# Kernel tuning notes

Hardware: AMD Instinct MI355X
Metric: run time of the kernel (lower is better)

## Reference

```python
import jax, jax.numpy as jnp
import numpy as np

B, S, E, H = 4, 2048, 1024, 16
D = E // H  # key_size


def setup_inputs() -> dict:
    key = jax.random.key(0)
    ks = jax.random.split(key, 6)
    s = 1.0 / np.sqrt(E)
    return {
        "X": jax.random.normal(ks[0], (B, S, E), dtype=jnp.float32),
        "Wq": jax.random.uniform(ks[1], (E, E), jnp.float32, -s, s),
        "Wk": jax.random.uniform(ks[2], (E, E), jnp.float32, -s, s),
        "Wv": jax.random.uniform(ks[3], (E, E), jnp.float32, -s, s),
        "Wo": jax.random.uniform(ks[4], (E, E), jnp.float32, -s, s),
        "bo": jax.random.uniform(ks[5], (E,), jnp.float32, -s, s),
    }


def reference(X, Wq, Wk, Wv, Wo, bo):
    # Linear layers: y = x @ W^T (torch convention), no bias for q/k/v
    def split(x):  # [B,S,E] -> [B,H,S,D]
        return x.reshape(B, S, H, D).transpose(0, 2, 1, 3)

    q = split(X @ Wq.T)
    k = split(X @ Wk.T)
    v = split(X @ Wv.T)
    scale = jnp.asarray(np.sqrt(D), dtype=X.dtype)
    scores = jnp.einsum("bhqd,bhkd->bhqk", q, k) / scale
    probs = jax.nn.softmax(scores, axis=-1)
    ctx = jnp.einsum("bhqk,bhkd->bhqd", probs, v)
    out = ctx.transpose(0, 2, 1, 3).reshape(B, S, E)
    return out @ Wo.T + bo
```

## Files before the change

kernel.cpp:

```cpp
#include <hip/hip_runtime.h>
#include <hip/hip_bf16.h>

typedef short bf16x8 __attribute__((ext_vector_type(8)));
typedef float f32x4  __attribute__((ext_vector_type(4)));

__device__ __forceinline__ short f2bf(float f) {
    union { float f; unsigned u; } x; x.f = f;
    unsigned r = x.u + 0x7fffu + ((x.u >> 16) & 1u);
    return (short)(r >> 16);
}

__device__ __forceinline__ unsigned rbits(float f) {
    union { float f; unsigned u; } x; x.f = f;
    return x.u + 0x8000u;
}
__device__ __forceinline__ int pack2(float a, float b) {
    return (int)__builtin_amdgcn_perm(rbits(b), rbits(a), 0x07060302u);
}

__device__ __forceinline__ f32x4 mfma32k(bf16x8 a, bf16x8 b, f32x4 c) {
    return __builtin_amdgcn_mfma_f32_16x16x32_bf16(a, b, c, 0, 0, 0);
}

#define GLDS16(g, l)                                                            \
    __builtin_amdgcn_global_load_lds(                                           \
        (const __attribute__((address_space(1))) void*)(g),                     \
        (__attribute__((address_space(3))) void*)(l), 16, 0, 0)

static constexpr int Bb = 4, Ss = 2048, Ee = 1024, Hh = 16, Dd = 64;
static constexpr int Mrows = Bb * Ss;
static constexpr float CL2 = 0.1803368801111204f;

__global__ void cvt_all(const float* __restrict__ X,  const float* __restrict__ Wq,
                        const float* __restrict__ Wk, const float* __restrict__ Wv,
                        const float* __restrict__ Wo,
                        short* __restrict__ Xb, short* __restrict__ Wqk,
                        short* __restrict__ Wvb, short* __restrict__ Wob) {
    int bid = blockIdx.x;
    const float* src; short* dst; int off; float scale = 1.0f;
    if (bid < 8192) {
        src = X; dst = Xb; off = bid * 1024;
    } else {
        int wsel = (bid - 8192) >> 10;
        off = ((bid - 8192) & 1023) * 1024;
        if      (wsel == 0) { src = Wq; dst = Wqk;                scale = CL2; }
        else if (wsel == 1) { src = Wk; dst = Wqk + Ee * Ee; }
        else if (wsel == 2) { src = Wv; dst = Wvb; }
        else                { src = Wo; dst = Wob; }
    }
    int i = off + threadIdx.x * 4;
    float4 v = *(const float4*)(src + i);
    short4 o;
    o.x = f2bf(v.x * scale); o.y = f2bf(v.y * scale);
    o.z = f2bf(v.z * scale); o.w = f2bf(v.w * scale);
    *(short4*)(dst + i) = o;
}

__global__ __launch_bounds__(512, 2)
void gemm_fused(const short* __restrict__ A0, const short* __restrict__ B0,
                short* __restrict__ C0,
                const short* __restrict__ A1, const short* __restrict__ B1,
                short* __restrict__ C1) {
    __shared__ __align__(16) short lds[65536];
    const int t = threadIdx.x, l = t & 63, wv = t >> 6;
    const int lane16 = l & 15, quad = l >> 4;
    const int wm = wv >> 2, wn = wv & 3;

    int bid = blockIdx.x;
    int wg = (bid & 7) * 48 + (bid >> 3);
    const short *A, *Bm; short* C;
    int bm, bn, ldc; bool perm;
    if (wg < 256) { bm = wg & 31; bn = wg >> 5; A = A0; Bm = B0; C = C0; ldc = 2048; perm = false; }
    else { int v = wg - 256; bm = v & 3; bn = v >> 2; A = A1; Bm = B1; C = C1; ldc = 8192; perm = true; }

    const short* Ab = A  + (size_t)bm * 256 * 1024;
    const short* Bp = Bm + (size_t)bn * 256 * 1024;

    const int grow = t >> 3;
    const int lsl  = ((t & 7) ^ ((t >> 3) & 7)) * 8;
    const short* gA = Ab + (size_t)grow * 1024 + lsl;
    const short* gB = Bp + (size_t)grow * 1024 + lsl;

#define STAGE8(gsrc, matOff, half, j, T, buf)                                   \
    GLDS16((gsrc) + ((half) * 128 + (j) * 64) * 1024 + (T) * 64,                \
           lds + (buf) * 32768 + (matOff) + (half) * 8192 + (j) * 4096 + wv * 512)

    const int fsw0 = ((quad)     ^ (lane16 & 7)) * 8;
    const int fsw1 = ((quad + 4) ^ (lane16 & 7)) * 8;
    const int aoff = (wm * 128 + lane16) * 64;
    const int boff = (wn * 64  + lane16) * 64;

    f32x4 acc[8][4] = {};

    STAGE8(gA, 0,     0, 0, 0, 0); STAGE8(gA, 0,     0, 1, 0, 0);
    STAGE8(gA, 0,     1, 0, 0, 0); STAGE8(gA, 0,     1, 1, 0, 0);
    STAGE8(gB, 16384, 0, 0, 0, 0); STAGE8(gB, 16384, 0, 1, 0, 0);
    STAGE8(gB, 16384, 1, 0, 0, 0); STAGE8(gB, 16384, 1, 1, 0, 0);
    STAGE8(gA, 0,     0, 0, 1, 1); STAGE8(gA, 0,     0, 1, 1, 1);
    asm volatile("s_waitcnt vmcnt(2)" ::: "memory");
    __builtin_amdgcn_s_barrier();

#define ARD(MI0)                                                                \
    a0 = *(const bf16x8*)(sAc + aoff + (MI0) * 1024 + fsw0);                    \
    a1 = *(const bf16x8*)(sAc + aoff + (MI0) * 1024 + fsw1);                    \
    a2 = *(const bf16x8*)(sAc + aoff + ((MI0) + 1) * 1024 + fsw0);              \
    a3 = *(const bf16x8*)(sAc + aoff + ((MI0) + 1) * 1024 + fsw1);

#define MFQ(MI0)                                                                \
    __builtin_amdgcn_s_setprio(1);                                              \
    _Pragma("unroll")                                                           \
    for (int nj = 0; nj < 4; ++nj) {                                            \
        acc[MI0][nj]       = mfma32k(a0, bf[nj][0], acc[MI0][nj]);              \
        acc[MI0][nj]       = mfma32k(a1, bf[nj][1], acc[MI0][nj]);              \
        acc[(MI0) + 1][nj] = mfma32k(a2, bf[nj][0], acc[(MI0) + 1][nj]);        \
        acc[(MI0) + 1][nj] = mfma32k(a3, bf[nj][1], acc[(MI0) + 1][nj]);        \
    }                                                                           \
    __builtin_amdgcn_s_setprio(0);

    for (int T = 0; T < 16; ++T) {
        const int cur = T & 1, nxt = cur ^ 1;
        const short* sAc = lds + cur * 32768;
        const short* sBc = sAc + 16384;
        bf16x8 bf[4][2];
#pragma unroll
        for (int nj = 0; nj < 4; ++nj) {
            bf[nj][0] = *(const bf16x8*)(sBc + boff + nj * 1024 + fsw0);
            bf[nj][1] = *(const bf16x8*)(sBc + boff + nj * 1024 + fsw1);
        }
        bf16x8 a0, a1, a2, a3;
        ARD(0)
        if (T < 15) { STAGE8(gA, 0, 1, 0, T + 1, nxt); STAGE8(gA, 0, 1, 1, T + 1, nxt); }
        __builtin_amdgcn_s_barrier();
        MFQ(0)
        __builtin_amdgcn_s_barrier();
        ARD(2)
        if (T < 15) { STAGE8(gB, 16384, 0, 0, T + 1, nxt); STAGE8(gB, 16384, 0, 1, T + 1, nxt); }
        __builtin_amdgcn_s_barrier();
        MFQ(2)
        __builtin_amdgcn_s_barrier();
        ARD(4)
        if (T < 15) { STAGE8(gB, 16384, 1, 0, T + 1, nxt); STAGE8(gB, 16384, 1, 1, T + 1, nxt); }
        __builtin_amdgcn_s_barrier();
        MFQ(4)
        __builtin_amdgcn_s_barrier();
        ARD(6)
        __builtin_amdgcn_s_barrier();
        MFQ(6)
        __builtin_amdgcn_s_barrier();
        if (T < 14) {
            STAGE8(gA, 0, 0, 0, T + 2, cur); STAGE8(gA, 0, 0, 1, T + 2, cur);
            asm volatile("s_waitcnt vmcnt(2)" ::: "memory");
            __builtin_amdgcn_s_barrier();
        } else if (T == 14) {
            asm volatile("s_waitcnt vmcnt(0)" ::: "memory");
            __builtin_amdgcn_s_barrier();
        }
    }
#undef ARD
#undef MFQ
#undef STAGE8

    const int sEven = (lane16 >> 2) * 8 + (lane16 & 3);
#pragma unroll
    for (int mi = 0; mi < 8; ++mi)
#pragma unroll
        for (int nj = 0; nj < 4; ++nj) {
            int row = bm * 256 + wm * 128 + mi * 16 + quad * 4;
            int col = bn * 256 + wn * 64 + nj * 16 + lane16;
            if (perm) col = (col & ~31) | (sEven + (nj & 1) * 4);
#pragma unroll
            for (int r = 0; r < 4; ++r)
                C[(size_t)(row + r) * ldc + col] = f2bf(acc[mi][nj][r]);
        }
}

__global__ __launch_bounds__(256, 3)
void gemm_out(const short* __restrict__ A, const short* __restrict__ Bm,
              float* __restrict__ C, const float* __restrict__ bias) {
    __shared__ __align__(16) short sA[128 * 32];
    __shared__ __align__(16) short sB[128 * 32];
    const int t = threadIdx.x, w = t >> 6, l = t & 63;
    const int lane16 = l & 15, quad = l >> 4;
    const int wm = (w >> 1) * 64, wn = (w & 1) * 64;
    const int bm = blockIdx.x, bn = blockIdx.y;

    f32x4 acc[4][4] = {};
    const short* Ab  = A  + (size_t)bm * 128 * 1024;
    const short* Bbp = Bm + (size_t)bn * 128 * 1024;
    const int s0 = w * 64 + l;
    const int ldsOff = (w * 64) * 8;

    for (int k0 = 0; k0 < 1024; k0 += 32) {
#pragma unroll
        for (int p = 0; p < 2; ++p) {
            int s = p * 256 + s0;
            int row = s >> 2, cs = s & 3;
            GLDS16(Ab + (size_t)row * 1024 + k0 + cs * 8, sA + p * 2048 + ldsOff);
            GLDS16(Bbp + (size_t)row * 1024 + k0 + cs * 8, sB + p * 2048 + ldsOff);
        }
        __syncthreads();
        bf16x8 af[4], bfr[4];
#pragma unroll
        for (int i = 0; i < 4; ++i) {
            af[i]  = *(const bf16x8*)(sA + (wm + i * 16 + lane16) * 32 + quad * 8);
            bfr[i] = *(const bf16x8*)(sB + (wn + i * 16 + lane16) * 32 + quad * 8);
        }
#pragma unroll
        for (int i = 0; i < 4; ++i)
#pragma unroll
            for (int j = 0; j < 4; ++j)
                acc[i][j] = mfma32k(af[i], bfr[j], acc[i][j]);
        __syncthreads();
    }

#pragma unroll
    for (int i = 0; i < 4; ++i)
#pragma unroll
        for (int j = 0; j < 4; ++j) {
            int row = bm * 128 + wm + i * 16 + quad * 4;
            int col = bn * 128 + wn + j * 16 + lane16;
            float bv = bias[col];
#pragma unroll
            for (int r = 0; r < 4; ++r)
                C[(size_t)(row + r) * 1024 + col] = acc[i][j][r] + bv;
        }
}

__global__ __launch_bounds__(256, 4)
void attn_kernel(const short* __restrict__ QK, const short* __restrict__ VT,
                 short* __restrict__ CTX, int bh0) {
    __shared__ __align__(16) short sK[8192];
    __shared__ __align__(16) short sV[8192];
    const int t = threadIdx.x, w = t >> 6, l = t & 63;
    const int lane16 = l & 15, quad = l >> 4;
    const int bh = blockIdx.x + bh0, qt = blockIdx.y;
    const int b = bh >> 4, h = bh & 15;

    const int qx8 = (quad ^ ((lane16 >> 1) & 3)) * 8;

    const short* Qb = QK + ((size_t)(b * 2048 + qt * 128)) * 2048 + h * 64;
    const short* Vb = VT + ((size_t)(h * 64)) * 8192 + (size_t)b * 2048;
    const int ldsOff = (w * 64) * 8;

    int off_kq[4], off_v[4];
#pragma unroll
    for (int p = 0; p < 4; ++p) {
        int c = p * 256 + t;
        int sw = ((c & 3) ^ ((c >> 3) & 3)) * 8;
        off_kq[p] = ((c >> 2) & 127) * 2048 + (c >> 9) * 32 + sw;
        off_v[p]  = ((c >> 2) & 63) * 8192 + (c >> 8) * 32 + sw;
    }

#pragma unroll
    for (int p = 0; p < 4; ++p)
        GLDS16(Qb + off_kq[p], sK + p * 2048 + ldsOff);
    __syncthreads();
    bf16x8 qf[2][2];
#pragma unroll
    for (int mt = 0; mt < 2; ++mt)
#pragma unroll
        for (int ks = 0; ks < 2; ++ks)
            qf[mt][ks] = *(const bf16x8*)(sK + ks * 4096 + (w * 32 + mt * 16 + lane16) * 32 + qx8);
    __syncthreads();

    const short one = (short)0x3F80;
    const bf16x8 ONE8 = {one, one, one, one, one, one, one, one};
    f32x4 lacc[2] = {};
    f32x4 o[2][4] = {};

    const short* kptr = QK + ((size_t)(b * 2048)) * 2048 + 1024 + h * 64;
    const short* vptr = Vb;

    auto QKB = [&](int a, f32x4 (&sc)[2][2]) {
        __builtin_amdgcn_s_setprio(1);
#pragma unroll
        for (int sub = 0; sub < 2; ++sub) {
            int nt = a * 2 + sub;
            bf16x8 kf0 = *(const bf16x8*)(sK + (nt * 16 + lane16) * 32 + qx8);
            bf16x8 kf1 = *(const bf16x8*)(sK + 4096 + (nt * 16 + lane16) * 32 + qx8);
#pragma unroll
            for (int mt = 0; mt < 2; ++mt) {
                f32x4 z = {};
                z = mfma32k(kf0, qf[mt][0], z);
                z = mfma32k(kf1, qf[mt][1], z);
                sc[mt][sub] = z;
            }
        }
        __builtin_amdgcn_s_setprio(0);
    };
    auto PVB = [&](int a, f32x4 (&sc)[2][2]) {
        bf16x8 pf[2];
#pragma unroll
        for (int mt = 0; mt < 2; ++mt) {
            union { int i[4]; bf16x8 v; } u;
#pragma unroll
            for (int sub = 0; sub < 2; ++sub) {
                f32x4 e;
#pragma unroll
                for (int r = 0; r < 4; ++r)
                    e[r] = __builtin_amdgcn_exp2f(sc[mt][sub][r]);
                u.i[sub * 2]     = pack2(e[0], e[1]);
                u.i[sub * 2 + 1] = pack2(e[2], e[3]);
            }
            pf[mt] = u.v;
        }
        __builtin_amdgcn_s_setprio(1);
#pragma unroll
        for (int mt = 0; mt < 2; ++mt)
            lacc[mt] = mfma32k(pf[mt], ONE8, lacc[mt]);
#pragma unroll
        for (int dt = 0; dt < 4; ++dt) {
            bf16x8 vf = *(const bf16x8*)(sV + a * 2048 + (dt * 16 + lane16) * 32 + qx8);
#pragma unroll
            for (int mt = 0; mt < 2; ++mt)
                o[mt][dt] = mfma32k(pf[mt], vf, o[mt][dt]);
        }
        __builtin_amdgcn_s_setprio(0);
    };

    for (int kt = 0; kt < 16; ++kt) {
#pragma unroll
        for (int p = 0; p < 4; ++p)
            GLDS16(kptr + off_kq[p], sK + p * 2048 + ldsOff);
#pragma unroll
        for (int p = 0; p < 4; ++p)
            GLDS16(vptr + off_v[p], sV + p * 2048 + ldsOff);
        kptr += (size_t)128 * 2048;
        vptr += 128;
        __syncthreads();

        f32x4 scA[2][2], scB[2][2];
        QKB(0, scA);
        QKB(1, scB);  PVB(0, scA);
        QKB(2, scA);  PVB(1, scB);
        QKB(3, scB);  PVB(2, scA);
                      PVB(3, scB);
        __syncthreads();
    }

#pragma unroll
    for (int mt = 0; mt < 2; ++mt)
#pragma unroll
        for (int r = 0; r < 4; ++r) {
            float inv = 1.0f / lacc[mt][r];
            int row = b * 2048 + qt * 128 + w * 32 + mt * 16 + quad * 4 + r;
#pragma unroll
            for (int dt = 0; dt < 4; ++dt)
                CTX[(size_t)row * 1024 + h * 64 + dt * 16 + lane16] = f2bf(o[mt][dt][r] * inv);
        }
}

extern "C" void kernel_launch(void* const* d_in, const int* in_sizes, int n_in,
                              void* d_out, int out_size, void* d_ws, size_t ws_size,
                              hipStream_t stream) {
    const float* X  = (const float*)d_in[0];
    const float* Wq = (const float*)d_in[1];
    const float* Wk = (const float*)d_in[2];
    const float* Wv = (const float*)d_in[3];
    const float* Wo = (const float*)d_in[4];
    const float* bo = (const float*)d_in[5];
    float* out = (float*)d_out;

    char* ws = (char*)d_ws;
    constexpr size_t OFF_XB  = 0;
    constexpr size_t OFF_WQK = OFF_XB  + (size_t)Mrows * Ee * 2;
    constexpr size_t OFF_WV  = OFF_WQK + (size_t)2 * Ee * Ee * 2;
    constexpr size_t OFF_WO  = OFF_WV  + (size_t)Ee * Ee * 2;
    constexpr size_t OFF_QK  = OFF_WO  + (size_t)Ee * Ee * 2;
    constexpr size_t OFF_VT  = OFF_QK  + (size_t)Mrows * 2048 * 2;
    constexpr size_t OFF_CTX = OFF_VT  + (size_t)Ee * Mrows * 2;
    short* Xb   = (short*)(ws + OFF_XB);
    short* Wqk  = (short*)(ws + OFF_WQK);
    short* Wvb  = (short*)(ws + OFF_WV);
    short* Wob  = (short*)(ws + OFF_WO);
    short* QKb  = (short*)(ws + OFF_QK);
    short* VTb  = (short*)(ws + OFF_VT);
    short* CTX  = (short*)(ws + OFF_CTX);

    cvt_all<<<12288, 256, 0, stream>>>(X, Wq, Wk, Wv, Wo, Xb, Wqk, Wvb, Wob);

    gemm_fused<<<384, 512, 0, stream>>>(Xb, Wqk, QKb, Wvb, Xb, VTb);

    attn_kernel<<<dim3(32, Ss / 128), 256, 0, stream>>>(QKb, VTb, CTX, 0);
    attn_kernel<<<dim3(32, Ss / 128), 256, 0, stream>>>(QKb, VTb, CTX, 32);

    gemm_out<<<dim3(Mrows / 128, Ee / 128), 256, 0, stream>>>(CTX, Wob, out, bo);
}
```

Measured before the change: 258.2 us.

## Rebalance projection GEMMs into 256 uniform blocks and pipeline output GEMM

The fused QK/V projection kernel now launches 256 blocks. Each block computes one 256x256 QK tile and then one 256x128 V^T tile through a new shared double-buffered pipelined helper, replacing the uneven 384-block schedule. The output projection GEMM is rewritten onto the same 256x128 pipelined LDS path with 512 threads and setprio, instead of a simple single-buffered 128x128 loop. The two half-batch attention launches are merged into one launch. Each projection block now does more sequential work, which could raise per-block latency and hurt tail behaviour.

Result: faster. 248.7 us (-3.7%).

```diff
diff --git a/kernel.cpp b/kernel.cpp
--- a/kernel.cpp
+++ b/kernel.cpp
@@ -56,6 +56,96 @@
     *(short4*)(dst + i) = o;
 }
 
+__device__ __forceinline__ void gemm_pipe_256x128(
+    short* lds, const short* hA, const short* hB,
+    int wv, int lane16, int wn, int fsw0, int fsw1, int aoff,
+    f32x4 (&acc)[8][2])
+{
+#define STG(gsrc, matOff, half, j, T, buf)                                      \
+    GLDS16((gsrc) + ((half) * 128 + (j) * 64) * 1024 + (T) * 64,                \
+           lds + (buf) * 32768 + (matOff) + (half) * 8192 + (j) * 4096 + wv * 512)
+
+    STG(hA, 0,     0, 0, 0, 0); STG(hA, 0,     0, 1, 0, 0);
+    STG(hA, 0,     1, 0, 0, 0); STG(hA, 0,     1, 1, 0, 0);
+    STG(hB, 16384, 0, 0, 0, 0); STG(hB, 16384, 0, 1, 0, 0);
+    STG(hA, 0,     0, 0, 1, 1); STG(hA, 0,     0, 1, 1, 1);
+    asm volatile("s_waitcnt vmcnt(2)" ::: "memory");
+    __builtin_amdgcn_s_barrier();
+
+    const int bvoff = (wn * 32 + lane16) * 64;
+    for (int T = 0; T < 16; ++T) {
+        const int cur = T & 1, nxt = cur ^ 1;
+        const short* sAc = lds + cur * 32768;
+        const short* sBc = sAc + 16384;
+        bf16x8 bb[2][2];
+#pragma unroll
+        for (int nj = 0; nj < 2; ++nj) {
+            bb[nj][0] = *(const bf16x8*)(sBc + bvoff + nj * 1024 + fsw0);
+            bb[nj][1] = *(const bf16x8*)(sBc + bvoff + nj * 1024 + fsw1);
+        }
+        bf16x8 a0, a1, a2, a3, a4, a5, a6, a7;
+        a0 = *(const bf16x8*)(sAc + aoff + 0 * 1024 + fsw0);
+        a1 = *(const bf16x8*)(sAc + aoff + 0 * 1024 + fsw1);
+        a2 = *(const bf16x8*)(sAc + aoff + 1 * 1024 + fsw0);
+        a3 = *(const bf16x8*)(sAc + aoff + 1 * 1024 + fsw1);
+        a4 = *(const bf16x8*)(sAc + aoff + 2 * 1024 + fsw0);
+        a5 = *(const bf16x8*)(sAc + aoff + 2 * 1024 + fsw1);
+        a6 = *(const bf16x8*)(sAc + aoff + 3 * 1024 + fsw0);
+        a7 = *(const bf16x8*)(sAc + aoff + 3 * 1024 + fsw1);
+        if (T < 15) {
+            STG(hA, 0,     1, 0, T + 1, nxt); STG(hA, 0,     1, 1, T + 1, nxt);
+            STG(hB, 16384, 0, 0, T + 1, nxt); STG(hB, 16384, 0, 1, T + 1, nxt);
+        }
+        __builtin_amdgcn_s_barrier();
+        __builtin_amdgcn_s_setprio(1);
+#pragma unroll
+        for (int nj = 0; nj < 2; ++nj) {
+            acc[0][nj] = mfma32k(a0, bb[nj][0], acc[0][nj]);
+            acc[0][nj] = mfma32k(a1, bb[nj][1], acc[0][nj]);
+            acc[1][nj] = mfma32k(a2, bb[nj][0], acc[1][nj]);
+            acc[1][nj] = mfma32k(a3, bb[nj][1], acc[1][nj]);
+            acc[2][nj] = mfma32k(a4, bb[nj][0], acc[2][nj]);
+            acc[2][nj] = mfma32k(a5, bb[nj][1], acc[2][nj]);
+            acc[3][nj] = mfma32k(a6, bb[nj][0], acc[3][nj]);
+            acc[3][nj] = mfma32k(a7, bb[nj][1], acc[3][nj]);
+        }
+        __builtin_amdgcn_s_setprio(0);
+        __builtin_amdgcn_s_barrier();
+        a0 = *(const bf16x8*)(sAc + aoff + 4 * 1024 + fsw0);
+        a1 = *(const bf16x8*)(sAc + aoff + 4 * 1024 + fsw1);
+        a2 = *(const bf16x8*)(sAc + aoff + 5 * 1024 + fsw0);
+        a3 = *(const bf16x8*)(sAc + aoff + 5 * 1024 + fsw1);
+        a4 = *(const bf16x8*)(sAc + aoff + 6 * 1024 + fsw0);
+        a5 = *(const bf16x8*)(sAc + aoff + 6 * 1024 + fsw1);
+        a6 = *(const bf16x8*)(sAc + aoff + 7 * 1024 + fsw0);
+        a7 = *(const bf16x8*)(sAc + aoff + 7 * 1024 + fsw1);
+        __builtin_amdgcn_s_barrier();
+        __builtin_amdgcn_s_setprio(1);
+#pragma unroll
+        for (int nj = 0; nj < 2; ++nj) {
+            acc[4][nj] = mfma32k(a0, bb[nj][0], acc[4][nj]);
+            acc[4][nj] = mfma32k(a1, bb[nj][1], acc[4][nj]);
+            acc[5][nj] = mfma32k(a2, bb[nj][0], acc[5][nj]);
+            acc[5][nj] = mfma32k(a3, bb[nj][1], acc[5][nj]);
+            acc[6][nj] = mfma32k(a4, bb[nj][0], acc[6][nj]);
+            acc[6][nj] = mfma32k(a5, bb[nj][1], acc[6][nj]);
+            acc[7][nj] = mfma32k(a6, bb[nj][0], acc[7][nj]);
+            acc[7][nj] = mfma32k(a7, bb[nj][1], acc[7][nj]);
+        }
+        __builtin_amdgcn_s_setprio(0);
+        __builtin_amdgcn_s_barrier();
+        if (T < 14) {
+            STG(hA, 0, 0, 0, T + 2, cur); STG(hA, 0, 0, 1, T + 2, cur);
+            asm volatile("s_waitcnt vmcnt(2)" ::: "memory");
+            __builtin_amdgcn_s_barrier();
+        } else if (T == 14) {
+            asm volatile("s_waitcnt vmcnt(0)" ::: "memory");
+            __builtin_amdgcn_s_barrier();
+        }
+    }
+#undef STG
+}
+
 __global__ __launch_bounds__(512, 2)
 void gemm_fused(const short* __restrict__ A0, const short* __restrict__ B0,
                 short* __restrict__ C0,
@@ -67,19 +157,13 @@
     const int wm = wv >> 2, wn = wv & 3;
 
     int bid = blockIdx.x;
-    int wg = (bid & 7) * 48 + (bid >> 3);
-    const short *A, *Bm; short* C;
-    int bm, bn, ldc; bool perm;
-    if (wg < 256) { bm = wg & 31; bn = wg >> 5; A = A0; Bm = B0; C = C0; ldc = 2048; perm = false; }
-    else { int v = wg - 256; bm = v & 3; bn = v >> 2; A = A1; Bm = B1; C = C1; ldc = 8192; perm = true; }
-
-    const short* Ab = A  + (size_t)bm * 256 * 1024;
-    const short* Bp = Bm + (size_t)bn * 256 * 1024;
+    int wg = (bid & 7) * 32 + (bid >> 3);
+    const int bm = wg & 31, bn = wg >> 5;
 
     const int grow = t >> 3;
     const int lsl  = ((t & 7) ^ ((t >> 3) & 7)) * 8;
-    const short* gA = Ab + (size_t)grow * 1024 + lsl;
-    const short* gB = Bp + (size_t)grow * 1024 + lsl;
+    const short* gA = A0 + (size_t)(bm * 256 + grow) * 1024 + lsl;
+    const short* gB = B0 + (size_t)(bn * 256 + grow) * 1024 + lsl;
 
 #define STAGE8(gsrc, matOff, half, j, T, buf)                                   \
     GLDS16((gsrc) + ((half) * 128 + (j) * 64) * 1024 + (T) * 64,                \
@@ -160,69 +244,71 @@
 #undef MFQ
 #undef STAGE8
 
-    const int sEven = (lane16 >> 2) * 8 + (lane16 & 3);
 #pragma unroll
     for (int mi = 0; mi < 8; ++mi)
 #pragma unroll
         for (int nj = 0; nj < 4; ++nj) {
             int row = bm * 256 + wm * 128 + mi * 16 + quad * 4;
             int col = bn * 256 + wn * 64 + nj * 16 + lane16;
-            if (perm) col = (col & ~31) | (sEven + (nj & 1) * 4);
 #pragma unroll
             for (int r = 0; r < 4; ++r)
-                C[(size_t)(row + r) * ldc + col] = f2bf(acc[mi][nj][r]);
-        }
-}
-
-__global__ __launch_bounds__(256, 3)
+                C0[(size_t)(row + r) * 2048 + col] = f2bf(acc[mi][nj][r]);
+        }
+
+    const int vbm = wg & 3, vbn = wg >> 2;
+    const short* hA = A1 + (size_t)(vbm * 256 + grow) * 1024 + lsl;
+    const short* hB = B1 + (size_t)(vbn * 128 + grow) * 1024 + lsl;
+    f32x4 accB[8][2] = {};
+    gemm_pipe_256x128(lds, hA, hB, wv, lane16, wn, fsw0, fsw1, aoff, accB);
+
+    const int sEven = (lane16 >> 2) * 8 + (lane16 & 3);
+#pragma unroll
+    for (int mi = 0; mi < 8; ++mi)
+#pragma unroll
+        for (int nj = 0; nj < 2; ++nj) {
+            int row = vbm * 256 + wm * 128 + mi * 16 + quad * 4;
+            int col = vbn * 128 + wn * 32 + nj * 16 + lane16;
+            col = (col & ~31) | (sEven + (nj & 1) * 4);
+#pragma unroll
+            for (int r = 0; r < 4; ++r)
+                C1[(size_t)(row + r) * 8192 + col] = f2bf(accB[mi][nj][r]);
+        }
+}
+
+__global__ __launch_bounds__(512, 2)
 void gemm_out(const short* __restrict__ A, const short* __restrict__ Bm,
               float* __restrict__ C, const float* __restrict__ bias) {
-    __shared__ __align__(16) short sA[128 * 32];
-    __shared__ __align__(16) short sB[128 * 32];
-    const int t = threadIdx.x, w = t >> 6, l = t & 63;
+    __shared__ __align__(16) short lds[65536];
+    const int t = threadIdx.x, l = t & 63, wv = t >> 6;
     const int lane16 = l & 15, quad = l >> 4;
-    const int wm = (w >> 1) * 64, wn = (w & 1) * 64;
-    const int bm = blockIdx.x, bn = blockIdx.y;
-
-    f32x4 acc[4][4] = {};
-    const short* Ab  = A  + (size_t)bm * 128 * 1024;
-    const short* Bbp = Bm + (size_t)bn * 128 * 1024;
-    const int s0 = w * 64 + l;
-    const int ldsOff = (w * 64) * 8;
-
-    for (int k0 = 0; k0 < 1024; k0 += 32) {
-#pragma unroll
-        for (int p = 0; p < 2; ++p) {
-            int s = p * 256 + s0;
-            int row = s >> 2, cs = s & 3;
-            GLDS16(Ab + (size_t)row * 1024 + k0 + cs * 8, sA + p * 2048 + ldsOff);
-            GLDS16(Bbp + (size_t)row * 1024 + k0 + cs * 8, sB + p * 2048 + ldsOff);
-        }
-        __syncthreads();
-        bf16x8 af[4], bfr[4];
-#pragma unroll
-        for (int i = 0; i < 4; ++i) {
-            af[i]  = *(const bf16x8*)(sA + (wm + i * 16 + lane16) * 32 + quad * 8);
-            bfr[i] = *(const bf16x8*)(sB + (wn + i * 16 + lane16) * 32 + quad * 8);
-        }
-#pragma unroll
-        for (int i = 0; i < 4; ++i)
-#pragma unroll
-            for (int j = 0; j < 4; ++j)
-                acc[i][j] = mfma32k(af[i], bfr[j], acc[i][j]);
-        __syncthreads();
-    }
-
-#pragma unroll
-    for (int i = 0; i < 4; ++i)
-#pragma unroll
-        for (int j = 0; j < 4; ++j) {
-            int row = bm * 128 + wm + i * 16 + quad * 4;
-            int col = bn * 128 + wn + j * 16 + lane16;
+    const int wm = wv >> 2, wn = wv & 3;
+
+    int bid = blockIdx.x;
+    int wg = (bid & 7) * 32 + (bid >> 3);
+    const int bm = wg >> 3, bn = wg & 7;
+
+    const int grow = t >> 3;
+    const int lsl  = ((t & 7) ^ ((t >> 3) & 7)) * 8;
+    const short* hA = A  + (size_t)(bm * 256 + grow) * 1024 + lsl;
+    const short* hB = Bm + (size_t)(bn * 128 + grow) * 1024 + lsl;
+
+    const int fsw0 = ((quad)     ^ (lane16 & 7)) * 8;
+    const int fsw1 = ((quad + 4) ^ (lane16 & 7)) * 8;
+    const int aoff = (wm * 128 + lane16) * 64;
+
+    f32x4 acc[8][2] = {};
+    gemm_pipe_256x128(lds, hA, hB, wv, lane16, wn, fsw0, fsw1, aoff, acc);
+
+#pragma unroll
+    for (int mi = 0; mi < 8; ++mi)
+#pragma unroll
+        for (int nj = 0; nj < 2; ++nj) {
+            int row = bm * 256 + wm * 128 + mi * 16 + quad * 4;
+            int col = bn * 128 + wn * 32 + nj * 16 + lane16;
             float bv = bias[col];
 #pragma unroll
             for (int r = 0; r < 4; ++r)
-                C[(size_t)(row + r) * 1024 + col] = acc[i][j][r] + bv;
+                C[(size_t)(row + r) * 1024 + col] = acc[mi][nj][r] + bv;
         }
 }
 
@@ -379,10 +465,9 @@
 
     cvt_all<<<12288, 256, 0, stream>>>(X, Wq, Wk, Wv, Wo, Xb, Wqk, Wvb, Wob);
 
-    gemm_fused<<<384, 512, 0, stream>>>(Xb, Wqk, QKb, Wvb, Xb, VTb);
-
-    attn_kernel<<<dim3(32, Ss / 128), 256, 0, stream>>>(QKb, VTb, CTX, 0);
-    attn_kernel<<<dim3(32, Ss / 128), 256, 0, stream>>>(QKb, VTb, CTX, 32);
-
-    gemm_out<<<dim3(Mrows / 128, Ee / 128), 256, 0, stream>>>(CTX, Wob, out, bo);
-}
+    gemm_fused<<<256, 512, 0, stream>>>(Xb, Wqk, QKb, Wvb, Xb, VTb);
+
+    attn_kernel<<<dim3(Bb * Hh, Ss / 128), 256, 0, stream>>>(QKb, VTb, CTX, 0);
+
+    gemm_out<<<256, 512, 0, stream>>>(CTX, Wob, out, bo);
+}
```
